# Optimization experiments

Hardware: AMD Instinct MI355X
Metric: run time of the kernel (lower is better)

The kernel has to match this reference:

```python
import jax, jax.numpy as jnp
import numpy as np

B, S, IN, OUT, H, L, NH, STEPS = 256, 128, 64, 64, 1024, 2, 4, 16
HD = H // NH


def setup_inputs() -> dict:
    key = jax.random.key(0)
    ks = iter(jax.random.split(key, 32))
    std_h = 1.0 / np.sqrt(H)

    def u(k, shape, std):
        return jax.random.uniform(k, shape, jnp.float32, -std, std)

    inp = {"x": jax.random.normal(next(ks), (B, S, IN), jnp.float32)}
    # LSTM cells: stacked gate weights, gate order (i, f, g, o); y = x@Wx + h@Wh + b
    for name, din in (("e0", IN), ("e1", H), ("d0", OUT), ("d1", H)):
        inp[name + "_Wx"] = u(next(ks), (din, 4 * H), std_h)
        inp[name + "_Wh"] = u(next(ks), (H, 4 * H), std_h)
        inp[name + "_b"] = u(next(ks), (4 * H,), std_h)
    # attention linears (x@W + b convention)
    for name in ("Wq", "Wk", "Wv", "Wo"):
        inp[name] = u(next(ks), (H, H), std_h)
    for name in ("bq", "bk", "bv", "bo"):
        inp[name] = u(next(ks), (H,), std_h)
    inp["fc_W"] = u(next(ks), (2 * H, H), 1.0 / np.sqrt(2 * H))
    inp["fc_b"] = u(next(ks), (H,), 1.0 / np.sqrt(2 * H))
    inp["out_W"] = u(next(ks), (H, OUT), std_h)
    inp["out_b"] = u(next(ks), (OUT,), std_h)
    return inp


def _cell(x_t, h, c, Wx, Wh, b):
    z = x_t @ Wx + h @ Wh + b  # [B, 4H]
    i, f, g, o = jnp.split(z, 4, axis=-1)
    c = jax.nn.sigmoid(f) * c + jax.nn.sigmoid(i) * jnp.tanh(g)
    h = jax.nn.sigmoid(o) * jnp.tanh(c)
    return h, c


def _lstm_seq(x, Wx, Wh, b):
    # x: [B, T, D] -> outputs [B, T, H], final (h, c)
    h0 = jnp.zeros((x.shape[0], H), x.dtype)
    def step(carry, xt):
        h, c = carry
        h, c = _cell(xt, h, c, Wx, Wh, b)
        return (h, c), h
    (h, c), ys = jax.lax.scan(step, (h0, h0), jnp.swapaxes(x, 0, 1))
    return jnp.swapaxes(ys, 0, 1), h, c


def reference(x, e0_Wx, e0_Wh, e0_b, e1_Wx, e1_Wh, e1_b,
              d0_Wx, d0_Wh, d0_b, d1_Wx, d1_Wh, d1_b,
              Wq, bq, Wk, bk, Wv, bv, Wo, bo, fc_W, fc_b, out_W, out_b):
    # encoder: 2-layer manual LSTM (dropout=0, eval)
    y0, h0, c0 = _lstm_seq(x, e0_Wx, e0_Wh, e0_b)
    enc_out, h1, c1 = _lstm_seq(y0, e1_Wx, e1_Wh, e1_b)

    # K/V projections of encoder outputs (constant across decoder steps)
    Kp = (enc_out @ Wk + bk).reshape(B, S, NH, HD)
    Vp = (enc_out @ Wv + bv).reshape(B, S, NH, HD)
    scale = float(HD) ** 0.5

    def dstep(carry, _):
        dh0, dc0, dh1, dc1, xin = carry
        dh0, dc0 = _cell(xin, dh0, dc0, d0_Wx, d0_Wh, d0_b)
        dh1, dc1 = _cell(dh0, dh1, dc1, d1_Wx, d1_Wh, d1_b)
        q = (dh1 @ Wq + bq).reshape(B, NH, HD)
        scores = jnp.einsum('bnd,bsnd->bns', q, Kp) / scale
        w = jax.nn.softmax(scores, axis=-1)
        ctx = jnp.einsum('bns,bsnd->bnd', w, Vp).reshape(B, H)
        attn = ctx @ Wo + bo
        comb = jax.nn.relu(jnp.concatenate([dh1, attn], axis=-1) @ fc_W + fc_b)
        out = comb @ out_W + out_b  # [B, OUT]
        return (dh0, dc0, dh1, dc1, out), out

    init = (h0, c0, h1, c1, jnp.zeros((B, OUT), x.dtype))
    _, preds = jax.lax.scan(dstep, init, None, length=STEPS)
    return jnp.swapaxes(preds, 0, 1)  # [B, STEPS, OUT]
```

## Files before the change

kernel.cpp:

```cpp
#include <hip/hip_runtime.h>
#include <math.h>

typedef _Float16 h8 __attribute__((ext_vector_type(8)));
typedef _Float16 h4 __attribute__((ext_vector_type(4)));
typedef float f16v __attribute__((ext_vector_type(16)));

#define HPS 262144
#define XPS 2097152
#define IPS 16384

__device__ __forceinline__ float4 ld4(const float* p) { return *(const float4*)p; }
__device__ __forceinline__ float sigf(float x) { return 1.0f / (1.0f + expf(-x)); }
__device__ __forceinline__ float bf2f(unsigned short u) { return __uint_as_float(((unsigned)u) << 16); }
__device__ __forceinline__ float rdin(const void* p, size_t i, int bf) {
  return bf ? bf2f(((const unsigned short*)p)[i]) : ((const float*)p)[i];
}

__global__ void detect_dtype(const unsigned short* __restrict__ probe, int n, int* flag) {
  __shared__ int cnt;
  if (threadIdx.x == 0) cnt = 0;
  __syncthreads();
  int c = 0;
  for (int i = threadIdx.x; i < n; i += 256) {
    int e = (probe[i] >> 7) & 0xFF;
    if (e >= 100 && e <= 126) c++;
  }
  atomicAdd(&cnt, c);
  __syncthreads();
  if (threadIdx.x == 0) *flag = (cnt > (n * 3) / 4) ? 1 : 0;
}

__global__ void cvt_f32(const void* __restrict__ in, float* __restrict__ out, int n,
                        const int* __restrict__ flag) {
  int bf = *flag;
  int i = blockIdx.x * 256 + threadIdx.x;
  if (i < n) out[i] = rdin(in, i, bf);
}

__global__ void tsplit(const void* __restrict__ in, int N,
                       _Float16* __restrict__ outHi, _Float16* __restrict__ outLo,
                       int ldo, int kOff, int pOff, const int* __restrict__ flag) {
  __shared__ float tile[32][33];
  int bf = *flag;
  int kb = blockIdx.x * 32, nb = blockIdx.y * 32;
  for (int r = threadIdx.y; r < 32; r += 8)
    tile[threadIdx.x][r] = rdin(in, (size_t)(kb + r) * N + nb + threadIdx.x, bf);
  __syncthreads();
  for (int r = threadIdx.y; r < 32; r += 8) {
    float v = tile[r][threadIdx.x];
    _Float16 hi = (_Float16)v;
    _Float16 lo = (_Float16)(v - (float)hi);
    size_t o = (size_t)(pOff + nb + r) * ldo + kOff + kb + threadIdx.x;
    outHi[o] = hi; outLo[o] = lo;
  }
}

__global__ void f2h_kernel(const void* __restrict__ in, _Float16* __restrict__ out, int n,
                           const int* __restrict__ flag) {
  int bf = *flag;
  int i = blockIdx.x * 1024 + threadIdx.x * 4;
  if (i < n) {
    float vv[4];
#pragma unroll
    for (int k = 0; k < 4; ++k) vv[k] = rdin(in, i + k, bf);
    h4 hv, lv;
#pragma unroll
    for (int k = 0; k < 4; ++k) { hv[k] = (_Float16)vv[k]; lv[k] = (_Float16)(vv[k] - (float)hv[k]); }
    *(h4*)(out + i) = hv;
    *(h4*)(out + n + i) = lv;
  }
}

__global__ void sentinel_kernel(float* out, float v) { out[0] = v; }

__device__ __forceinline__ void gemm_tile(
    const _Float16* __restrict__ A0, int lda0, int aps0,
    const _Float16* __restrict__ A1, int lda1, int aps1, int ksplit,
    const _Float16* __restrict__ WTh, const _Float16* __restrict__ WTl, int ldw,
    int pbase, int c0, int c1, int mbase,
    float* __restrict__ zp, int zld, _Float16* Bs ) {
  const int tid = threadIdx.x;
  const int wv = tid >> 6, lane = tid & 63;
  const int l31 = lane & 31, lhi = lane >> 5;

  f16v acc00 = {}, acc01 = {}, acc10 = {}, acc11 = {};

  const int r0 = mbase + wv * 64 + l31;
  const int r1 = r0 + 32;
  const _Float16* a0b0 = A0 + (size_t)r0 * lda0;
  const _Float16* a1b0 = A1 + (size_t)r0 * lda1;
  const _Float16* a0b1 = A0 + (size_t)r1 * lda0;
  const _Float16* a1b1 = A1 + (size_t)r1 * lda1;

  const int spl = tid >> 7;
  const int sidx = tid & 127;
  const int sp = sidx >> 1;
  const int skh = (sidx & 1) << 4;
  const _Float16* srow = (spl ? WTl : WTh) + (size_t)(pbase + sp) * ldw + skh;
  _Float16* sdst = Bs + ((size_t)(spl * 64 + sp)) * 40 + skh;

  for (int c = c0; c < c1; ++c) {
    int k0 = c << 5;
    const _Float16* s = srow + k0;
    float4 v0 = *(const float4*)(s);
    float4 v1 = *(const float4*)(s + 8);
    __syncthreads();
    *(float4*)(sdst) = v0;
    *(float4*)(sdst + 8) = v1;
    __syncthreads();
#pragma unroll
    for (int sub = 0; sub < 2; ++sub) {
      int ks = k0 + sub * 16 + lhi * 8;
      const _Float16 *pa0, *pa1; int ap;
      if (ks < ksplit) { pa0 = a0b0 + ks; pa1 = a0b1 + ks; ap = aps0; }
      else { int kk = ks - ksplit; pa0 = a1b0 + kk; pa1 = a1b1 + kk; ap = aps1; }
      h8 af0h = *(const h8*)pa0;
      h8 af0l = *(const h8*)(pa0 + ap);
      h8 af1h = *(const h8*)pa1;
      h8 af1l = *(const h8*)(pa1 + ap);
      int kl = sub * 16 + lhi * 8;
      h8 b0h = *(const h8*)(Bs + (size_t)(l31) * 40 + kl);
      h8 b0l = *(const h8*)(Bs + (size_t)(64 + l31) * 40 + kl);
      h8 b1h = *(const h8*)(Bs + (size_t)(32 + l31) * 40 + kl);
      h8 b1l = *(const h8*)(Bs + (size_t)(96 + l31) * 40 + kl);
      acc00 = __builtin_amdgcn_mfma_f32_32x32x16_f16(af0h, b0h, acc00, 0, 0, 0);
      acc00 = __builtin_amdgcn_mfma_f32_32x32x16_f16(af0h, b0l, acc00, 0, 0, 0);
      acc00 = __builtin_amdgcn_mfma_f32_32x32x16_f16(af0l, b0h, acc00, 0, 0, 0);
      acc01 = __builtin_amdgcn_mfma_f32_32x32x16_f16(af0h, b1h, acc01, 0, 0, 0);
      acc01 = __builtin_amdgcn_mfma_f32_32x32x16_f16(af0h, b1l, acc01, 0, 0, 0);
      acc01 = __builtin_amdgcn_mfma_f32_32x32x16_f16(af0l, b1h, acc01, 0, 0, 0);
      acc10 = __builtin_amdgcn_mfma_f32_32x32x16_f16(af1h, b0h, acc10, 0, 0, 0);
      acc10 = __builtin_amdgcn_mfma_f32_32x32x16_f16(af1h, b0l, acc10, 0, 0, 0);
      acc10 = __builtin_amdgcn_mfma_f32_32x32x16_f16(af1l, b0h, acc10, 0, 0, 0);
      acc11 = __builtin_amdgcn_mfma_f32_32x32x16_f16(af1h, b1h, acc11, 0, 0, 0);
      acc11 = __builtin_amdgcn_mfma_f32_32x32x16_f16(af1h, b1l, acc11, 0, 0, 0);
      acc11 = __builtin_amdgcn_mfma_f32_32x32x16_f16(af1l, b1h, acc11, 0, 0, 0);
    }
  }

#pragma unroll
  for (int mi = 0; mi < 2; ++mi) {
#pragma unroll
    for (int ni = 0; ni < 2; ++ni) {
      f16v av = (mi == 0) ? (ni == 0 ? acc00 : acc01) : (ni == 0 ? acc10 : acc11);
      int col = pbase + ni * 32 + l31;
#pragma unroll
      for (int r = 0; r < 16; ++r) {
        int row = mbase + wv * 64 + mi * 32 + (r & 3) + ((r >> 2) * 8) + lhi * 4;
        zp[(size_t)row * zld + col] = av[r];
      }
    }
  }
}

__global__ __launch_bounds__(256) void enc_gemm(int t,
    const _Float16* xh, const _Float16* h0, const _Float16* h1,
    const _Float16* wt0h, const _Float16* wt0l,
    const _Float16* wt1h, const _Float16* wt1l,
    const _Float16* wtkvh, const _Float16* wtkvl,
    float* z0, float* z1, float* kvz) {
  __shared__ _Float16 Bs[2 * 64 * 40];
  int blk = blockIdx.x;
  if (blk < 128) {
    if (t > 127) return;
    int pg = blk & 63, kq = blk >> 6;
    gemm_tile(xh + (size_t)t * 64, 8192, XPS, h0, 1024, HPS, 64, wt0h, wt0l, 1088,
              pg * 64, kq * 17, kq * 17 + 17, 0, z0 + (size_t)kq * 1048576, 4096, Bs);
  } else if (blk < 256) {
    if (t < 1 || t > 128) return;
    int w = blk - 128, pg = w & 63, kq = w >> 6;
    gemm_tile(h0, 1024, HPS, h1, 1024, HPS, 1024, wt1h, wt1l, 2048,
              pg * 64, kq * 32, kq * 32 + 32, 0, z1 + (size_t)kq * 1048576, 4096, Bs);
  } else {
    if (t < 2) return;
    int w = blk - 256, pg = w & 31, kq = w >> 5;
    gemm_tile(h1, 1024, HPS, h1, 1024, HPS, 1024, wtkvh, wtkvl, 1024,
              pg * 64, kq * 16, kq * 16 + 16, 0, kvz + (size_t)kq * 524288, 2048, Bs);
  }
}

__global__ __launch_bounds__(256) void gemm_k(
    const _Float16* A0, int lda0, int aps0,
    const _Float16* A1, int lda1, int aps1, int ksplit,
    const _Float16* WTh, const _Float16* WTl, int ldw,
    int npg, int nkq, int tot, float* zp, int zld) {
  __shared__ _Float16 Bs[2 * 64 * 40];
  int pg = blockIdx.x % npg, kq = blockIdx.x / npg;
  int c0 = (tot * kq) / nkq, c1 = (tot * (kq + 1)) / nkq;
  gemm_tile(A0, lda0, aps0, A1, lda1, aps1, ksplit, WTh, WTl, ldw,
            pg * 64, c0, c1, 0, zp + (size_t)kq * 256 * zld, zld, Bs);
}

__device__ __forceinline__ void gates_body(const float* __restrict__ zp, int nparts,
    const float* __restrict__ bias, float* __restrict__ c,
    _Float16* __restrict__ h, int blk) {
  int e = blk * 1024 + threadIdx.x * 4;
  int b = e >> 10, j = e & 1023;
  size_t zrow = (size_t)b * 4096;
  float4 vi = ld4(bias + j), vf = ld4(bias + 1024 + j), vg = ld4(bias + 2048 + j), vo = ld4(bias + 3072 + j);
  for (int q = 0; q < nparts; ++q) {
    const float* zq = zp + (size_t)q * 1048576 + zrow;
    float4 t;
    t = ld4(zq + j);        vi.x += t.x; vi.y += t.y; vi.z += t.z; vi.w += t.w;
    t = ld4(zq + 1024 + j); vf.x += t.x; vf.y += t.y; vf.z += t.z; vf.w += t.w;
    t = ld4(zq + 2048 + j); vg.x += t.x; vg.y += t.y; vg.z += t.z; vg.w += t.w;
    t = ld4(zq + 3072 + j); vo.x += t.x; vo.y += t.y; vo.z += t.z; vo.w += t.w;
  }
  float* cp = c + (size_t)b * 1024 + j;
  float4 cv = ld4(cp);
  float zi[4] = {vi.x, vi.y, vi.z, vi.w}, zf[4] = {vf.x, vf.y, vf.z, vf.w};
  float zg[4] = {vg.x, vg.y, vg.z, vg.w}, zo[4] = {vo.x, vo.y, vo.z, vo.w};
  float cc[4] = {cv.x, cv.y, cv.z, cv.w};
  float hn[4];
#pragma unroll
  for (int k = 0; k < 4; ++k) {
    float ii = sigf(zi[k]), ff = sigf(zf[k]), gg = tanhf(zg[k]), oo = sigf(zo[k]);
    float cn = ff * cc[k] + ii * gg;
    cc[k] = cn;
    hn[k] = oo * tanhf(cn);
  }
  float4 co; co.x = cc[0]; co.y = cc[1]; co.z = cc[2]; co.w = cc[3];
  *(float4*)cp = co;
  h4 hv, lv;
#pragma unroll
  for (int k = 0; k < 4; ++k) { hv[k] = (_Float16)hn[k]; lv[k] = (_Float16)(hn[k] - (float)hv[k]); }
  *(h4*)(h + (size_t)b * 1024 + j) = hv;
  *(h4*)(h + HPS + (size_t)b * 1024 + j) = lv;
}

__global__ void enc_gates(int t, const float* z0, const float* z1, const float* kvz,
                          const float* b0, const float* b1,
                          const float* bk, const float* bv,
                          float* c0, float* c1, _Float16* h0, _Float16* h1,
                          _Float16* Kp, _Float16* Vp) {
  int blk = blockIdx.x;
  if (blk < 256) {
    if (t > 127) return;
    gates_body(z0, 2, b0, c0, h0, blk);
  } else if (blk < 512) {
    if (t < 1 || t > 128) return;
    gates_body(z1, 2, b1, c1, h1, blk - 256);
  } else {
    if (t < 2) return;
    int e = (blk - 512) * 1024 + threadIdx.x * 4;
    int b = e >> 11, col = e & 2047;
    const float* bb = (col < 1024) ? (bk + col) : (bv + col - 1024);
    float4 v = ld4(bb);
    for (int q = 0; q < 2; ++q) {
      float4 tt = ld4(kvz + (size_t)q * 524288 + e);
      v.x += tt.x; v.y += tt.y; v.z += tt.z; v.w += tt.w;
    }
    _Float16* dst = (col < 1024) ? Kp : Vp;
    int cc = (col < 1024) ? col : col - 1024;
    h4 hv; hv[0] = (_Float16)v.x; hv[1] = (_Float16)v.y; hv[2] = (_Float16)v.z; hv[3] = (_Float16)v.w;
    *(h4*)(dst + (size_t)(b * 128 + (t - 2)) * 1024 + cc) = hv;
  }
}

__global__ void dec_gates(const float* zp, int nparts, const float* bias,
                          float* c, _Float16* h) {
  gates_body(zp, nparts, bias, c, h, blockIdx.x);
}

__global__ void reduce_act(const float* __restrict__ zp, int nparts,
                           const float* __restrict__ bias, _Float16* __restrict__ out, int relu) {
  int e = blockIdx.x * 1024 + threadIdx.x * 4;
  int j = e & 1023;
  float4 v = ld4(bias + j);
  for (int q = 0; q < nparts; ++q) {
    float4 t = ld4(zp + (size_t)q * 262144 + e);
    v.x += t.x; v.y += t.y; v.z += t.z; v.w += t.w;
  }
  if (relu) {
    v.x = fmaxf(v.x, 0.f); v.y = fmaxf(v.y, 0.f); v.z = fmaxf(v.z, 0.f); v.w = fmaxf(v.w, 0.f);
  }
  float vv[4] = {v.x, v.y, v.z, v.w};
  h4 hv, lv;
#pragma unroll
  for (int k = 0; k < 4; ++k) { hv[k] = (_Float16)vv[k]; lv[k] = (_Float16)(vv[k] - (float)hv[k]); }
  *(h4*)(out + e) = hv;
  *(h4*)(out + HPS + e) = lv;
}

__global__ void out_reduce(const float* __restrict__ op, const float* __restrict__ outb,
                           float* __restrict__ dout, _Float16* __restrict__ xin, int s) {
  int e = blockIdx.x * 1024 + threadIdx.x * 4;
  int b = e >> 6, o = e & 63;
  float4 v = ld4(outb + o);
  for (int q = 0; q < 16; ++q) {
    float4 t = ld4(op + (size_t)q * 16384 + e);
    v.x += t.x; v.y += t.y; v.z += t.z; v.w += t.w;
  }
  *(float4*)(dout + (size_t)(b * 16 + s) * 64 + o) = v;
  float vv[4] = {v.x, v.y, v.z, v.w};
  h4 hv, lv;
#pragma unroll
  for (int k = 0; k < 4; ++k) { hv[k] = (_Float16)vv[k]; lv[k] = (_Float16)(vv[k] - (float)hv[k]); }
  *(h4*)(xin + e) = hv;
  *(h4*)(xin + IPS + e) = lv;
}

__global__ void attn_kernel(const float* __restrict__ qp, const float* __restrict__ bq,
                            const _Float16* __restrict__ Kp, const _Float16* __restrict__ Vp,
                            _Float16* __restrict__ ctx) {
  int b = blockIdx.x >> 2, n = blockIdx.x & 3;
  __shared__ float qs[256];
  __shared__ float sw[128];
  int tid = threadIdx.x;
  float qv = bq[n * 256 + tid];
  for (int q = 0; q < 4; ++q) qv += qp[(size_t)q * 262144 + (size_t)b * 1024 + n * 256 + tid];
  qs[tid] = qv;
  __syncthreads();
  int w = tid >> 6, lane = tid & 63;
  for (int s = w; s < 128; s += 4) {
    const _Float16* kr = Kp + (size_t)(b * 128 + s) * 1024 + n * 256;
    float acc = 0.f;
#pragma unroll
    for (int d = 0; d < 4; ++d) acc += qs[lane + d * 64] * (float)kr[lane + d * 64];
    for (int off = 32; off; off >>= 1) acc += __shfl_down(acc, off);
    if (lane == 0) sw[s] = acc * 0.0625f;
  }
  __syncthreads();
  if (w == 0) {
    float a = sw[lane], bb = sw[lane + 64];
    float m = fmaxf(a, bb);
    for (int off = 32; off; off >>= 1) m = fmaxf(m, __shfl_down(m, off));
    m = __shfl(m, 0);
    float e1 = expf(a - m), e2 = expf(bb - m);
    float ss = e1 + e2;
    for (int off = 32; off; off >>= 1) ss += __shfl_down(ss, off);
    ss = __shfl(ss, 0);
    float inv = 1.0f / ss;
    sw[lane] = e1 * inv; sw[lane + 64] = e2 * inv;
  }
  __syncthreads();
  float acc = 0.f;
  const _Float16* vb = Vp + (size_t)b * 131072 + n * 256 + tid;
  for (int s2 = 0; s2 < 128; ++s2) acc += sw[s2] * (float)vb[(size_t)s2 * 1024];
  size_t idx = (size_t)b * 1024 + n * 256 + tid;
  _Float16 hi = (_Float16)acc;
  ctx[idx] = hi;
  ctx[HPS + idx] = (_Float16)(acc - (float)hi);
}

extern "C" void kernel_launch(void* const* d_in, const int* in_sizes, int n_in,
                              void* d_out, int out_size, void* d_ws, size_t ws_size,
                              hipStream_t stream) {
  const void* x     = d_in[0];
  const void* e0_Wx = d_in[1];
  const void* e0_Wh = d_in[2];
  const void* e0_b  = d_in[3];
  const void* e1_Wx = d_in[4];
  const void* e1_Wh = d_in[5];
  const void* e1_b  = d_in[6];
  const void* d0_Wx = d_in[7];
  const void* d0_Wh = d_in[8];
  const void* d0_b  = d_in[9];
  const void* d1_Wx = d_in[10];
  const void* d1_Wh = d_in[11];
  const void* d1_b  = d_in[12];
  const void* Wq = d_in[13];
  const void* Wk = d_in[14];
  const void* Wv = d_in[15];
  const void* Wo = d_in[16];
  const void* bq = d_in[17];
  const void* bk = d_in[18];
  const void* bv = d_in[19];
  const void* bo = d_in[20];
  const void* fc_W  = d_in[21];
  const void* fc_b  = d_in[22];
  const void* out_W = d_in[23];
  const void* out_b = d_in[24];

  char* p = (char*)d_ws;
  auto alloc = [&](size_t bytes) { char* r = p; p += (bytes + 255) & ~(size_t)255; return r; };

  int* flag = (int*)alloc(256);
  float* bias_arena = (float*)alloc(87040);
  float* c_e0b = bias_arena +     0;
  float* c_e1b = bias_arena +  4096;
  float* c_d0b = bias_arena +  8192;
  float* c_d1b = bias_arena + 12288;
  float* c_bq  = bias_arena + 16384;
  float* c_bk  = bias_arena + 17408;
  float* c_bv  = bias_arena + 18432;
  float* c_bo  = bias_arena + 19456;
  float* c_fcb = bias_arena + 20480;
  float* c_ob  = bias_arena + 21504;

  char* warena = alloc(68419584);
  _Float16* wt_e0h = (_Float16*)(warena);
  _Float16* wt_e0l = (_Float16*)(warena +  8912896);
  _Float16* wt_e1h = (_Float16*)(warena + 17825792);
  _Float16* wt_e1l = (_Float16*)(warena + 34603008);
  _Float16* wt_kvh = (_Float16*)(warena + 51380224);
  _Float16* wt_kvl = (_Float16*)(warena + 55574528);
  _Float16* xh     = (_Float16*)(warena + 59768832);
  _Float16* wt_d0h = (_Float16*)(warena);
  _Float16* wt_d0l = (_Float16*)(warena +  8912896);
  _Float16* wt_d1h = (_Float16*)(warena + 17825792);
  _Float16* wt_d1l = (_Float16*)(warena + 34603008);
  _Float16* wt_qh  = (_Float16*)(warena + 51380224);
  _Float16* wt_ql  = (_Float16*)(warena + 53477376);
  _Float16* wt_oh  = (_Float16*)(warena + 55574528);
  _Float16* wt_ol  = (_Float16*)(warena + 57671680);
  _Float16* wt_fch = (_Float16*)(warena + 59768832);
  _Float16* wt_fcl = (_Float16*)(warena + 63963136);
  _Float16* wt_outh= (_Float16*)(warena + 68157440);
  _Float16* wt_outl= (_Float16*)(warena + 68288512);

  char* zero0 = p;
  _Float16* h0 = (_Float16*)alloc(1048576);
  _Float16* h1 = (_Float16*)alloc(1048576);
  float* c0 = (float*)alloc(1048576);
  float* c1 = (float*)alloc(1048576);
  _Float16* xin = (_Float16*)alloc(65536);
  size_t zeroBytes = (size_t)(p - zero0);
  _Float16* Kp = (_Float16*)alloc(67108864);
  _Float16* Vp = (_Float16*)alloc(67108864);
  float* zarena = (float*)alloc(20971520);
  float* z0e = zarena;
  float* z1e = zarena + 2097152;
  float* kvz = zarena + 4194304;
  float* zdec = zarena;
  float* fcp = zarena;
  float* qp  = zarena + 2097152;
  float* op  = zarena + 3145728;
  _Float16* ctx    = (_Float16*)alloc(1048576);
  _Float16* attn_h = (_Float16*)alloc(1048576);
  _Float16* comb   = (_Float16*)alloc(1048576);

  if ((size_t)(p - (char*)d_ws) > ws_size) {
    sentinel_kernel<<<1, 1, 0, stream>>>((float*)d_out, 1.0e9f + (float)ws_size);
    return;
  }

  detect_dtype<<<1, 256, 0, stream>>>((const unsigned short*)e0_Wx, 16384, flag);
  cvt_f32<<<16, 256, 0, stream>>>(e0_b, c_e0b, 4096, flag);
  cvt_f32<<<16, 256, 0, stream>>>(e1_b, c_e1b, 4096, flag);
  cvt_f32<<<16, 256, 0, stream>>>(d0_b, c_d0b, 4096, flag);
  cvt_f32<<<16, 256, 0, stream>>>(d1_b, c_d1b, 4096, flag);
  cvt_f32<<<4, 256, 0, stream>>>(bq, c_bq, 1024, flag);
  cvt_f32<<<4, 256, 0, stream>>>(bk, c_bk, 1024, flag);
  cvt_f32<<<4, 256, 0, stream>>>(bv, c_bv, 1024, flag);
  cvt_f32<<<4, 256, 0, stream>>>(bo, c_bo, 1024, flag);
  cvt_f32<<<4, 256, 0, stream>>>(fc_b, c_fcb, 1024, flag);
  cvt_f32<<<1, 64, 0, stream>>>(out_b, c_ob, 64, flag);

  dim3 tb(32, 8);
  tsplit<<<dim3(2, 128), tb, 0, stream>>>(e0_Wx, 4096, wt_e0h, wt_e0l, 1088, 0, 0, flag);
  tsplit<<<dim3(32, 128), tb, 0, stream>>>(e0_Wh, 4096, wt_e0h, wt_e0l, 1088, 64, 0, flag);
  tsplit<<<dim3(32, 128), tb, 0, stream>>>(e1_Wx, 4096, wt_e1h, wt_e1l, 2048, 0, 0, flag);
  tsplit<<<dim3(32, 128), tb, 0, stream>>>(e1_Wh, 4096, wt_e1h, wt_e1l, 2048, 1024, 0, flag);
  tsplit<<<dim3(32, 32), tb, 0, stream>>>(Wk, 1024, wt_kvh, wt_kvl, 1024, 0, 0, flag);
  tsplit<<<dim3(32, 32), tb, 0, stream>>>(Wv, 1024, wt_kvh, wt_kvl, 1024, 0, 1024, flag);
  f2h_kernel<<<2048, 256, 0, stream>>>(x, xh, 2097152, flag);
  hipMemsetAsync(zero0, 0, zeroBytes, stream);

  for (int t = 0; t <= 129; ++t) {
    enc_gemm<<<320, 256, 0, stream>>>(t, xh, h0, h1, wt_e0h, wt_e0l, wt_e1h, wt_e1l,
                                      wt_kvh, wt_kvl, z0e, z1e, kvz);
    enc_gates<<<1024, 256, 0, stream>>>(t, z0e, z1e, kvz, c_e0b, c_e1b, c_bk, c_bv,
                                        c0, c1, h0, h1, Kp, Vp);
  }

  tsplit<<<dim3(2, 128), tb, 0, stream>>>(d0_Wx, 4096, wt_d0h, wt_d0l, 1088, 0, 0, flag);
  tsplit<<<dim3(32, 128), tb, 0, stream>>>(d0_Wh, 4096, wt_d0h, wt_d0l, 1088, 64, 0, flag);
  tsplit<<<dim3(32, 128), tb, 0, stream>>>(d1_Wx, 4096, wt_d1h, wt_d1l, 2048, 0, 0, flag);
  tsplit<<<dim3(32, 128), tb, 0, stream>>>(d1_Wh, 4096, wt_d1h, wt_d1l, 2048, 1024, 0, flag);
  tsplit<<<dim3(32, 32), tb, 0, stream>>>(Wq, 1024, wt_qh, wt_ql, 1024, 0, 0, flag);
  tsplit<<<dim3(32, 32), tb, 0, stream>>>(Wo, 1024, wt_oh, wt_ol, 1024, 0, 0, flag);
  tsplit<<<dim3(64, 32), tb, 0, stream>>>(fc_W, 1024, wt_fch, wt_fcl, 2048, 0, 0, flag);
  tsplit<<<dim3(32, 2), tb, 0, stream>>>(out_W, 64, wt_outh, wt_outl, 1024, 0, 0, flag);

  for (int s = 0; s < 16; ++s) {
    gemm_k<<<256, 256, 0, stream>>>(xin, 64, IPS, h0, 1024, HPS, 64,
                                    wt_d0h, wt_d0l, 1088, 64, 4, 34, zdec, 4096);
    dec_gates<<<256, 256, 0, stream>>>(zdec, 4, c_d0b, c0, h0);
    gemm_k<<<256, 256, 0, stream>>>(h0, 1024, HPS, h1, 1024, HPS, 1024,
                                    wt_d1h, wt_d1l, 2048, 64, 4, 64, zdec, 4096);
    dec_gates<<<256, 256, 0, stream>>>(zdec, 4, c_d1b, c1, h1);
    gemm_k<<<64, 256, 0, stream>>>(h1, 1024, HPS, h1, 1024, HPS, 1024,
                                   wt_qh, wt_ql, 1024, 16, 4, 32, qp, 1024);
    attn_kernel<<<1024, 256, 0, stream>>>(qp, c_bq, Kp, Vp, ctx);
    gemm_k<<<64, 256, 0, stream>>>(ctx, 1024, HPS, ctx, 1024, HPS, 1024,
                                   wt_oh, wt_ol, 1024, 16, 4, 32, qp, 1024);
    reduce_act<<<256, 256, 0, stream>>>(qp, 4, c_bo, attn_h, 0);
    gemm_k<<<128, 256, 0, stream>>>(h1, 1024, HPS, attn_h, 1024, HPS, 1024,
                                    wt_fch, wt_fcl, 2048, 16, 8, 64, fcp, 1024);
    reduce_act<<<256, 256, 0, stream>>>(fcp, 8, c_fcb, comb, 1);
    gemm_k<<<16, 256, 0, stream>>>(comb, 1024, HPS, comb, 1024, HPS, 1024,
                                   wt_outh, wt_outl, 1024, 1, 16, 32, op, 64);
    out_reduce<<<16, 256, 0, stream>>>(op, c_ob, (float*)d_out, xin, s);
  }
}
```

Baseline: 10.45 ms.

## Enlarge GEMM tiles to 256x128 with double-buffered LDS and fuse q/fc GEMMs

After: 13.07 ms. 1.25x slower.

```diff
diff --git a/kernel.cpp b/kernel.cpp
--- a/kernel.cpp
+++ b/kernel.cpp
@@ -8,6 +8,8 @@
 #define HPS 262144
 #define XPS 2097152
 #define IPS 16384
+#define BSTR 40
+#define BUFH (256 * BSTR)
 
 __device__ __forceinline__ float4 ld4(const float* p) { return *(const float4*)p; }
 __device__ __forceinline__ float sigf(float x) { return 1.0f / (1.0f + expf(-x)); }
@@ -77,105 +79,136 @@
     const _Float16* __restrict__ A0, int lda0, int aps0,
     const _Float16* __restrict__ A1, int lda1, int aps1, int ksplit,
     const _Float16* __restrict__ WTh, const _Float16* __restrict__ WTl, int ldw,
-    int pbase, int c0, int c1, int mbase,
+    int pbase, int c0, int c1,
     float* __restrict__ zp, int zld, _Float16* Bs ) {
   const int tid = threadIdx.x;
   const int wv = tid >> 6, lane = tid & 63;
+  const int wm = wv >> 1, wn = wv & 1;
   const int l31 = lane & 31, lhi = lane >> 5;
 
-  f16v acc00 = {}, acc01 = {}, acc10 = {}, acc11 = {};
-
-  const int r0 = mbase + wv * 64 + l31;
-  const int r1 = r0 + 32;
-  const _Float16* a0b0 = A0 + (size_t)r0 * lda0;
-  const _Float16* a1b0 = A1 + (size_t)r0 * lda1;
-  const _Float16* a0b1 = A0 + (size_t)r1 * lda0;
-  const _Float16* a1b1 = A1 + (size_t)r1 * lda1;
+  f16v acc[4][2] = {{{}, {}}, {{}, {}}, {{}, {}}, {{}, {}}};
+
+  const _Float16* a0p[4];
+  const _Float16* a1p[4];
+#pragma unroll
+  for (int rb = 0; rb < 4; ++rb) {
+    int r = wm * 128 + rb * 32 + l31;
+    a0p[rb] = A0 + (size_t)r * lda0;
+    a1p[rb] = A1 + (size_t)r * lda1;
+  }
 
   const int spl = tid >> 7;
-  const int sidx = tid & 127;
-  const int sp = sidx >> 1;
-  const int skh = (sidx & 1) << 4;
-  const _Float16* srow = (spl ? WTl : WTh) + (size_t)(pbase + sp) * ldw + skh;
-  _Float16* sdst = Bs + ((size_t)(spl * 64 + sp)) * 40 + skh;
-
-  for (int c = c0; c < c1; ++c) {
-    int k0 = c << 5;
-    const _Float16* s = srow + k0;
+  const int srow = tid & 127;
+  const _Float16* sbase = (spl ? WTl : WTh) + (size_t)(pbase + srow) * ldw;
+  const int sdoff = (spl * 128 + srow) * BSTR;
+
+  {
+    const _Float16* s = sbase + (c0 << 5);
     float4 v0 = *(const float4*)(s);
     float4 v1 = *(const float4*)(s + 8);
+    float4 v2 = *(const float4*)(s + 16);
+    float4 v3 = *(const float4*)(s + 24);
+    _Float16* d = Bs + sdoff;
+    *(float4*)(d) = v0;      *(float4*)(d + 8) = v1;
+    *(float4*)(d + 16) = v2; *(float4*)(d + 24) = v3;
+  }
+
+  int buf = 0;
+  for (int c = c0; c < c1; ++c) {
     __syncthreads();
-    *(float4*)(sdst) = v0;
-    *(float4*)(sdst + 8) = v1;
-    __syncthreads();
+    float4 n0, n1, n2, n3;
+    const bool more = (c + 1 < c1);
+    if (more) {
+      const _Float16* s = sbase + ((c + 1) << 5);
+      n0 = *(const float4*)(s);
+      n1 = *(const float4*)(s + 8);
+      n2 = *(const float4*)(s + 16);
+      n3 = *(const float4*)(s + 24);
+    }
+    const _Float16* bb = Bs + buf * BUFH;
 #pragma unroll
     for (int sub = 0; sub < 2; ++sub) {
-      int ks = k0 + sub * 16 + lhi * 8;
-      const _Float16 *pa0, *pa1; int ap;
-      if (ks < ksplit) { pa0 = a0b0 + ks; pa1 = a0b1 + ks; ap = aps0; }
-      else { int kk = ks - ksplit; pa0 = a1b0 + kk; pa1 = a1b1 + kk; ap = aps1; }
-      h8 af0h = *(const h8*)pa0;
-      h8 af0l = *(const h8*)(pa0 + ap);
-      h8 af1h = *(const h8*)pa1;
-      h8 af1l = *(const h8*)(pa1 + ap);
+      int ks = (c << 5) + sub * 16 + lhi * 8;
       int kl = sub * 16 + lhi * 8;
-      h8 b0h = *(const h8*)(Bs + (size_t)(l31) * 40 + kl);
-      h8 b0l = *(const h8*)(Bs + (size_t)(64 + l31) * 40 + kl);
-      h8 b1h = *(const h8*)(Bs + (size_t)(32 + l31) * 40 + kl);
-      h8 b1l = *(const h8*)(Bs + (size_t)(96 + l31) * 40 + kl);
-      acc00 = __builtin_amdgcn_mfma_f32_32x32x16_f16(af0h, b0h, acc00, 0, 0, 0);
-      acc00 = __builtin_amdgcn_mfma_f32_32x32x16_f16(af0h, b0l, acc00, 0, 0, 0);
-      acc00 = __builtin_amdgcn_mfma_f32_32x32x16_f16(af0l, b0h, acc00, 0, 0, 0);
-      acc01 = __builtin_amdgcn_mfma_f32_32x32x16_f16(af0h, b1h, acc01, 0, 0, 0);
-      acc01 = __builtin_amdgcn_mfma_f32_32x32x16_f16(af0h, b1l, acc01, 0, 0, 0);
-      acc01 = __builtin_amdgcn_mfma_f32_32x32x16_f16(af0l, b1h, acc01, 0, 0, 0);
-      acc10 = __builtin_amdgcn_mfma_f32_32x32x16_f16(af1h, b0h, acc10, 0, 0, 0);
-      acc10 = __builtin_amdgcn_mfma_f32_32x32x16_f16(af1h, b0l, acc10, 0, 0, 0);
-      acc10 = __builtin_amdgcn_mfma_f32_32x32x16_f16(af1l, b0h, acc10, 0, 0, 0);
-      acc11 = __builtin_amdgcn_mfma_f32_32x32x16_f16(af1h, b1h, acc11, 0, 0, 0);
-      acc11 = __builtin_amdgcn_mfma_f32_32x32x16_f16(af1h, b1l, acc11, 0, 0, 0);
-      acc11 = __builtin_amdgcn_mfma_f32_32x32x16_f16(af1l, b1h, acc11, 0, 0, 0);
+      h8 bh[2], bl[2];
+#pragma unroll
+      for (int cb = 0; cb < 2; ++cb) {
+        int colrow = wn * 64 + cb * 32 + l31;
+        bh[cb] = *(const h8*)(bb + (size_t)colrow * BSTR + kl);
+        bl[cb] = *(const h8*)(bb + (size_t)(128 + colrow) * BSTR + kl);
+      }
+      h8 ah[4], al[4];
+#pragma unroll
+      for (int rb = 0; rb < 4; ++rb) {
+        const _Float16* pa; int ap;
+        if (ks < ksplit) { pa = a0p[rb] + ks; ap = aps0; }
+        else             { pa = a1p[rb] + (ks - ksplit); ap = aps1; }
+        ah[rb] = *(const h8*)pa;
+        al[rb] = *(const h8*)(pa + ap);
+      }
+#pragma unroll
+      for (int rb = 0; rb < 4; ++rb)
+#pragma unroll
+        for (int cb = 0; cb < 2; ++cb)
+          acc[rb][cb] = __builtin_amdgcn_mfma_f32_32x32x16_f16(ah[rb], bh[cb], acc[rb][cb], 0, 0, 0);
+#pragma unroll
+      for (int rb = 0; rb < 4; ++rb)
+#pragma unroll
+        for (int cb = 0; cb < 2; ++cb)
+          acc[rb][cb] = __builtin_amdgcn_mfma_f32_32x32x16_f16(ah[rb], bl[cb], acc[rb][cb], 0, 0, 0);
+#pragma unroll
+      for (int rb = 0; rb < 4; ++rb)
+#pragma unroll
+        for (int cb = 0; cb < 2; ++cb)
+          acc[rb][cb] = __builtin_amdgcn_mfma_f32_32x32x16_f16(al[rb], bh[cb], acc[rb][cb], 0, 0, 0);
     }
-  }
-
-#pragma unroll
-  for (int mi = 0; mi < 2; ++mi) {
-#pragma unroll
-    for (int ni = 0; ni < 2; ++ni) {
-      f16v av = (mi == 0) ? (ni == 0 ? acc00 : acc01) : (ni == 0 ? acc10 : acc11);
-      int col = pbase + ni * 32 + l31;
+    if (more) {
+      _Float16* d = Bs + (buf ^ 1) * BUFH + sdoff;
+      *(float4*)(d) = n0;      *(float4*)(d + 8) = n1;
+      *(float4*)(d + 16) = n2; *(float4*)(d + 24) = n3;
+    }
+    buf ^= 1;
+  }
+
+#pragma unroll
+  for (int rb = 0; rb < 4; ++rb) {
+#pragma unroll
+    for (int cb = 0; cb < 2; ++cb) {
+      int col = pbase + wn * 64 + cb * 32 + l31;
 #pragma unroll
       for (int r = 0; r < 16; ++r) {
-        int row = mbase + wv * 64 + mi * 32 + (r & 3) + ((r >> 2) * 8) + lhi * 4;
-        zp[(size_t)row * zld + col] = av[r];
+        int row = wm * 128 + rb * 32 + (r & 3) + ((r >> 2) * 8) + lhi * 4;
+        zp[(size_t)row * zld + col] = acc[rb][cb][r];
       }
     }
   }
 }
 
-__global__ __launch_bounds__(256) void enc_gemm(int t,
+__global__ __launch_bounds__(256) void enc_gemm(int t, int l1kq,
     const _Float16* xh, const _Float16* h0, const _Float16* h1,
     const _Float16* wt0h, const _Float16* wt0l,
     const _Float16* wt1h, const _Float16* wt1l,
     const _Float16* wtkvh, const _Float16* wtkvl,
     float* z0, float* z1, float* kvz) {
-  __shared__ _Float16 Bs[2 * 64 * 40];
+  __shared__ _Float16 Bs[2 * BUFH];
   int blk = blockIdx.x;
-  if (blk < 128) {
+  int nl1 = 32 * l1kq;
+  if (blk < nl1) {
+    if (t < 1 || t > 128) return;
+    int pg = blk & 31, kq = blk >> 5;
+    int c0 = (64 * kq) / l1kq, c1 = (64 * (kq + 1)) / l1kq;
+    gemm_tile(h0, 1024, HPS, h1, 1024, HPS, 1024, wt1h, wt1l, 2048,
+              pg * 128, c0, c1, z1 + (size_t)kq * 1048576, 4096, Bs);
+  } else if (blk < nl1 + 64) {
     if (t > 127) return;
-    int pg = blk & 63, kq = blk >> 6;
+    int w = blk - nl1, pg = w & 31, kq = w >> 5;
     gemm_tile(xh + (size_t)t * 64, 8192, XPS, h0, 1024, HPS, 64, wt0h, wt0l, 1088,
-              pg * 64, kq * 17, kq * 17 + 17, 0, z0 + (size_t)kq * 1048576, 4096, Bs);
-  } else if (blk < 256) {
-    if (t < 1 || t > 128) return;
-    int w = blk - 128, pg = w & 63, kq = w >> 6;
-    gemm_tile(h0, 1024, HPS, h1, 1024, HPS, 1024, wt1h, wt1l, 2048,
-              pg * 64, kq * 32, kq * 32 + 32, 0, z1 + (size_t)kq * 1048576, 4096, Bs);
+              pg * 128, kq * 17, kq * 17 + 17, z0 + (size_t)kq * 1048576, 4096, Bs);
   } else {
     if (t < 2) return;
-    int w = blk - 256, pg = w & 31, kq = w >> 5;
+    int w = blk - nl1 - 64, pg = w & 15, kq = w >> 4;
     gemm_tile(h1, 1024, HPS, h1, 1024, HPS, 1024, wtkvh, wtkvl, 1024,
-              pg * 64, kq * 16, kq * 16 + 16, 0, kvz + (size_t)kq * 524288, 2048, Bs);
+              pg * 128, kq * 16, kq * 16 + 16, kvz + (size_t)kq * 524288, 2048, Bs);
   }
 }
 
@@ -183,12 +216,30 @@
     const _Float16* A0, int lda0, int aps0,
     const _Float16* A1, int lda1, int aps1, int ksplit,
     const _Float16* WTh, const _Float16* WTl, int ldw,
-    int npg, int nkq, int tot, float* zp, int zld) {
-  __shared__ _Float16 Bs[2 * 64 * 40];
-  int pg = blockIdx.x % npg, kq = blockIdx.x / npg;
+    int npg, int nkq, int tot, int kqoff, float* zp, int zld) {
+  __shared__ _Float16 Bs[2 * BUFH];
+  int pg = blockIdx.x % npg, kq = blockIdx.x / npg + kqoff;
   int c0 = (tot * kq) / nkq, c1 = (tot * (kq + 1)) / nkq;
   gemm_tile(A0, lda0, aps0, A1, lda1, aps1, ksplit, WTh, WTl, ldw,
-            pg * 64, c0, c1, 0, zp + (size_t)kq * 256 * zld, zld, Bs);
+            pg * 128, c0, c1, zp + (size_t)kq * 256 * zld, zld, Bs);
+}
+
+__global__ __launch_bounds__(256) void qfc_kernel(
+    const _Float16* h1,
+    const _Float16* wqh, const _Float16* wql,
+    const _Float16* wfh, const _Float16* wfl,
+    float* qp, float* fcp) {
+  __shared__ _Float16 Bs[2 * BUFH];
+  int blk = blockIdx.x;
+  if (blk < 32) {
+    int pg = blk & 7, kq = blk >> 3;
+    gemm_tile(h1, 1024, HPS, h1, 1024, HPS, 1024, wqh, wql, 1024,
+              pg * 128, kq * 8, kq * 8 + 8, qp + (size_t)kq * 262144, 1024, Bs);
+  } else {
+    int w = blk - 32, pg = w & 7, kq = w >> 3;
+    gemm_tile(h1, 1024, HPS, h1, 1024, HPS, 1024, wfh, wfl, 2048,
+              pg * 128, kq * 8, kq * 8 + 8, fcp + (size_t)kq * 262144, 1024, Bs);
+  }
 }
 
 __device__ __forceinline__ void gates_body(const float* __restrict__ zp, int nparts,
@@ -228,7 +279,7 @@
   *(h4*)(h + HPS + (size_t)b * 1024 + j) = lv;
 }
 
-__global__ void enc_gates(int t, const float* z0, const float* z1, const float* kvz,
+__global__ void enc_gates(int t, int l1parts, const float* z0, const float* z1, const float* kvz,
                           const float* b0, const float* b1,
                           const float* bk, const float* bv,
                           float* c0, float* c1, _Float16* h0, _Float16* h1,
@@ -239,7 +290,7 @@
     gates_body(z0, 2, b0, c0, h0, blk);
   } else if (blk < 512) {
     if (t < 1 || t > 128) return;
-    gates_body(z1, 2, b1, c1, h1, blk - 256);
+    gates_body(z1, l1parts, b1, c1, h1, blk - 256);
   } else {
     if (t < 2) return;
     int e = (blk - 512) * 1024 + threadIdx.x * 4;
@@ -288,7 +339,7 @@
   int b = e >> 6, o = e & 63;
   float4 v = ld4(outb + o);
   for (int q = 0; q < 16; ++q) {
-    float4 t = ld4(op + (size_t)q * 16384 + e);
+    float4 t = ld4(op + (size_t)q * 32768 + b * 128 + o);
     v.x += t.x; v.y += t.y; v.z += t.z; v.w += t.w;
   }
   *(float4*)(dout + (size_t)(b * 16 + s) * 64 + o) = v;
@@ -372,11 +423,40 @@
   const void* out_W = d_in[23];
   const void* out_b = d_in[24];
 
+  int l1parts = 4;
   char* p = (char*)d_ws;
-  auto alloc = [&](size_t bytes) { char* r = p; p += (bytes + 255) & ~(size_t)255; return r; };
-
-  int* flag = (int*)alloc(256);
-  float* bias_arena = (float*)alloc(87040);
+  int* flag; float* bias_arena; char* warena; char* zero0;
+  _Float16 *h0, *h1, *xin, *Kp, *Vp, *ctx, *attn_h, *comb;
+  float *c0, *c1; float* zarena;
+  size_t zeroBytes = 0;
+
+  for (int attempt = 0; attempt < 2; ++attempt) {
+    p = (char*)d_ws;
+    auto alloc = [&](size_t bytes) { char* r = p; p += (bytes + 255) & ~(size_t)255; return r; };
+    flag = (int*)alloc(256);
+    bias_arena = (float*)alloc(87040);
+    warena = alloc(68681728);
+    zero0 = p;
+    h0 = (_Float16*)alloc(1048576);
+    h1 = (_Float16*)alloc(1048576);
+    c0 = (float*)alloc(1048576);
+    c1 = (float*)alloc(1048576);
+    xin = (_Float16*)alloc(65536);
+    zeroBytes = (size_t)(p - zero0);
+    Kp = (_Float16*)alloc(67108864);
+    Vp = (_Float16*)alloc(67108864);
+    zarena = (float*)alloc((size_t)(3 + l1parts) * 4194304);
+    ctx    = (_Float16*)alloc(1048576);
+    attn_h = (_Float16*)alloc(1048576);
+    comb   = (_Float16*)alloc(1048576);
+    if ((size_t)(p - (char*)d_ws) <= ws_size) break;
+    l1parts = 2;
+  }
+  if ((size_t)(p - (char*)d_ws) > ws_size) {
+    sentinel_kernel<<<1, 1, 0, stream>>>((float*)d_out, 1.0e9f + (float)ws_size);
+    return;
+  }
+
   float* c_e0b = bias_arena +     0;
   float* c_e1b = bias_arena +  4096;
   float* c_d0b = bias_arena +  8192;
@@ -388,7 +468,6 @@
   float* c_fcb = bias_arena + 20480;
   float* c_ob  = bias_arena + 21504;
 
-  char* warena = alloc(68419584);
   _Float16* wt_e0h = (_Float16*)(warena);
   _Float16* wt_e0l = (_Float16*)(warena +  8912896);
   _Float16* wt_e1h = (_Float16*)(warena + 17825792);
@@ -407,33 +486,15 @@
   _Float16* wt_fch = (_Float16*)(warena + 59768832);
   _Float16* wt_fcl = (_Float16*)(warena + 63963136);
   _Float16* wt_outh= (_Float16*)(warena + 68157440);
-  _Float16* wt_outl= (_Float16*)(warena + 68288512);
-
-  char* zero0 = p;
-  _Float16* h0 = (_Float16*)alloc(1048576);
-  _Float16* h1 = (_Float16*)alloc(1048576);
-  float* c0 = (float*)alloc(1048576);
-  float* c1 = (float*)alloc(1048576);
-  _Float16* xin = (_Float16*)alloc(65536);
-  size_t zeroBytes = (size_t)(p - zero0);
-  _Float16* Kp = (_Float16*)alloc(67108864);
-  _Float16* Vp = (_Float16*)alloc(67108864);
-  float* zarena = (float*)alloc(20971520);
+  _Float16* wt_outl= (_Float16*)(warena + 68419584);
+
   float* z0e = zarena;
   float* z1e = zarena + 2097152;
-  float* kvz = zarena + 4194304;
+  float* kvz = z1e + (size_t)l1parts * 1048576;
   float* zdec = zarena;
   float* fcp = zarena;
   float* qp  = zarena + 2097152;
   float* op  = zarena + 3145728;
-  _Float16* ctx    = (_Float16*)alloc(1048576);
-  _Float16* attn_h = (_Float16*)alloc(1048576);
-  _Float16* comb   = (_Float16*)alloc(1048576);
-
-  if ((size_t)(p - (char*)d_ws) > ws_size) {
-    sentinel_kernel<<<1, 1, 0, stream>>>((float*)d_out, 1.0e9f + (float)ws_size);
-    return;
-  }
 
   detect_dtype<<<1, 256, 0, stream>>>((const unsigned short*)e0_Wx, 16384, flag);
   cvt_f32<<<16, 256, 0, stream>>>(e0_b, c_e0b, 4096, flag);
@@ -457,10 +518,12 @@
   f2h_kernel<<<2048, 256, 0, stream>>>(x, xh, 2097152, flag);
   hipMemsetAsync(zero0, 0, zeroBytes, stream);
 
+  int encBlocks = 32 * l1parts + 96;
   for (int t = 0; t <= 129; ++t) {
-    enc_gemm<<<320, 256, 0, stream>>>(t, xh, h0, h1, wt_e0h, wt_e0l, wt_e1h, wt_e1l,
-                                      wt_kvh, wt_kvl, z0e, z1e, kvz);
-    enc_gates<<<1024, 256, 0, stream>>>(t, z0e, z1e, kvz, c_e0b, c_e1b, c_bk, c_bv,
+    enc_gemm<<<encBlocks, 256, 0, stream>>>(t, l1parts, xh, h0, h1,
+                                            wt_e0h, wt_e0l, wt_e1h, wt_e1l,
+                                            wt_kvh, wt_kvl, z0e, z1e, kvz);
+    enc_gates<<<1024, 256, 0, stream>>>(t, l1parts, z0e, z1e, kvz, c_e0b, c_e1b, c_bk, c_bv,
                                         c0, c1, h0, h1, Kp, Vp);
   }
 
@@ -472,25 +535,26 @@
   tsplit<<<dim3(32, 32), tb, 0, stream>>>(Wo, 1024, wt_oh, wt_ol, 1024, 0, 0, flag);
   tsplit<<<dim3(64, 32), tb, 0, stream>>>(fc_W, 1024, wt_fch, wt_fcl, 2048, 0, 0, flag);
   tsplit<<<dim3(32, 2), tb, 0, stream>>>(out_W, 64, wt_outh, wt_outl, 1024, 0, 0, flag);
+  hipMemsetAsync(wt_outh + 65536, 0, 131072, stream);
+  hipMemsetAsync(wt_outl + 65536, 0, 131072, stream);
 
   for (int s = 0; s < 16; ++s) {
-    gemm_k<<<256, 256, 0, stream>>>(xin, 64, IPS, h0, 1024, HPS, 64,
-                                    wt_d0h, wt_d0l, 1088, 64, 4, 34, zdec, 4096);
+    gemm_k<<<128, 256, 0, stream>>>(xin, 64, IPS, h0, 1024, HPS, 64,
+                                    wt_d0h, wt_d0l, 1088, 32, 4, 34, 0, zdec, 4096);
     dec_gates<<<256, 256, 0, stream>>>(zdec, 4, c_d0b, c0, h0);
-    gemm_k<<<256, 256, 0, stream>>>(h0, 1024, HPS, h1, 1024, HPS, 1024,
-                                    wt_d1h, wt_d1l, 2048, 64, 4, 64, zdec, 4096);
+    gemm_k<<<128, 256, 0, stream>>>(h0, 1024, HPS, h1, 1024, HPS, 1024,
+                                    wt_d1h, wt_d1l, 2048, 32, 4, 64, 0, zdec, 4096);
     dec_gates<<<256, 256, 0, stream>>>(zdec, 4, c_d1b, c1, h1);
-    gemm_k<<<64, 256, 0, stream>>>(h1, 1024, HPS, h1, 1024, HPS, 1024,
-                                   wt_qh, wt_ql, 1024, 16, 4, 32, qp, 1024);
+    qfc_kernel<<<64, 256, 0, stream>>>(h1, wt_qh, wt_ql, wt_fch, wt_fcl, qp, fcp);
     attn_kernel<<<1024, 256, 0, stream>>>(qp, c_bq, Kp, Vp, ctx);
-    gemm_k<<<64, 256, 0, stream>>>(ctx, 1024, HPS, ctx, 1024, HPS, 1024,
-                                   wt_oh, wt_ol, 1024, 16, 4, 32, qp, 1024);
+    gemm_k<<<32, 256, 0, stream>>>(ctx, 1024, HPS, ctx, 1024, HPS, 1024,
+                                   wt_oh, wt_ol, 1024, 8, 4, 32, 0, qp, 1024);
     reduce_act<<<256, 256, 0, stream>>>(qp, 4, c_bo, attn_h, 0);
-    gemm_k<<<128, 256, 0, stream>>>(h1, 1024, HPS, attn_h, 1024, HPS, 1024,
-                                    wt_fch, wt_fcl, 2048, 16, 8, 64, fcp, 1024);
+    gemm_k<<<32, 256, 0, stream>>>(h1, 1024, HPS, attn_h, 1024, HPS, 1024,
+                                   wt_fch, wt_fcl, 2048, 8, 8, 64, 4, fcp, 1024);
     reduce_act<<<256, 256, 0, stream>>>(fcp, 8, c_fcb, comb, 1);
     gemm_k<<<16, 256, 0, stream>>>(comb, 1024, HPS, comb, 1024, HPS, 1024,
-                                   wt_outh, wt_outl, 1024, 1, 16, 32, op, 64);
+                                   wt_outh, wt_outl, 1024, 1, 16, 32, 0, op, 128);
     out_reduce<<<16, 256, 0, stream>>>(op, c_ob, (float*)d_out, xin, s);
   }
 }
```
